# Kernel tuning notes

Measured on AMD Instinct MI355X. Metric: run time of the kernel, lower is better.

## Reference

```python
import jax, jax.numpy as jnp
import numpy as np
from jax import lax

TAU = 2.0
VTH = 1.0
T = 4

def heaviside(x):
    return (x >= 0.0).astype(x.dtype)

def lif_step(v, x):
    # decay_input=False, v_reset=0: v <- v*(1-1/tau) + x ; hard reset to 0
    v = v * (1.0 - 1.0 / TAU) + x
    s = heaviside(v - VTH)
    v = v * (1.0 - s)
    return v, s

def setup_inputs() -> dict:
    key = jax.random.key(0)
    k = jax.random.split(key, 5)
    B, H, W3, W4 = 128, 64, 8, 32
    cc, N, O = 8, 512, 16
    flat = cc * H * W3 * W4  # 131072
    x = jax.random.normal(k[0], (B, 2, H, W3, W4), dtype=jnp.float32)
    w_conv = jax.random.normal(k[1], (cc, 2, 3, 3), dtype=jnp.float32) / np.sqrt(2 * 9)
    w1 = jax.random.normal(k[2], (N, flat), dtype=jnp.float32) / np.sqrt(flat)
    w2 = jax.random.normal(k[3], (N, N), dtype=jnp.float32) / np.sqrt(N)
    w_out = jax.random.normal(k[4], (O, N), dtype=jnp.float32) / np.sqrt(N)
    return {"x": x, "w_conv": w_conv, "w1": w1, "w2": w2, "w_out": w_out}

def reference(x, w_conv, w1, w2, w_out):
    B = x.shape[0]
    # input.reshape(B, C, -1, W4)
    xr = x.reshape(B, x.shape[1], -1, x.shape[4])  # (B, 2, 512, 32)
    conv_input = lax.conv_general_dilated(
        xr, w_conv, window_strides=(1, 1), padding="SAME",
        dimension_numbers=("NCHW", "OIHW", "NCHW"))  # (B, cc, 512, 32)

    # lifconv applied T times to the same conv_input with persistent state
    def conv_step(v, _):
        return lif_step(v, conv_input)
    _, conv_spikes = lax.scan(conv_step, jnp.zeros_like(conv_input), None, length=T)  # (T,B,cc,H',W')

    N = w1.shape[0]
    def fc_step(carry, s_conv):
        v1, v2 = carry
        z1 = s_conv.reshape(B, -1) @ w1.T
        v1, s1 = lif_step(v1, z1)
        z2 = s1 @ w2.T
        v2, s2 = lif_step(v2, z2)
        return (v1, v2), (s1, s2)

    v0 = (jnp.zeros((B, N), x.dtype), jnp.zeros((B, N), x.dtype))
    _, (s1_rec, s2_rec) = lax.scan(fc_step, v0, conv_spikes)  # (T,B,N) each

    out = s2_rec.mean(axis=0) @ w_out.T  # (B, O)
    conv_spk_rec = jnp.moveaxis(conv_spikes, 0, 1)   # (B,T,cc,H',W')
    input_spk_rec = jnp.moveaxis(s1_rec, 0, 1)       # (B,T,N)
    hidden_spk_rec = jnp.moveaxis(s2_rec, 0, 1)      # (B,T,N)
    return (out, conv_spk_rec, input_spk_rec, hidden_spk_rec)
```

## Files before the change

kernel.cpp:

```cpp
#include <hip/hip_runtime.h>
#include <stdint.h>


#define OFF_CONV  2048ll
#define OFF_IN    67110912ll
#define OFF_HID   67373056ll

typedef short bf16x8 __attribute__((ext_vector_type(8)));
typedef float f32x4  __attribute__((ext_vector_type(4)));

__device__ __forceinline__ unsigned short f2bf(float f) {
  unsigned u = __float_as_uint(f);
  u += 0x7FFFu + ((u >> 16) & 1u);
  return (unsigned short)(u >> 16);
}

__device__ __forceinline__ void expand2(unsigned x, unsigned& o0, unsigned& o1) {
  o0 = (x & 1u) * 0x3F80u | (x & 0x100u) * 0x3F8000u;
  unsigned y = x >> 16;
  o1 = (y & 1u) * 0x3F80u | (y & 0x100u) * 0x3F8000u;
}

__global__ __launch_bounds__(256) void conv_lif_kernel(
    const float* __restrict__ x, const float* __restrict__ wc,
    float* __restrict__ out, unsigned char* __restrict__ patt)
{
  __shared__ float wcs[144];
  int tid = threadIdx.x;
  if (tid < 144) wcs[tid] = wc[tid];
  __syncthreads();

  int idx = blockIdx.x * 256 + tid;
  int b   = idx >> 15;
  int k4  = idx & 32767;
  int co  = k4 >> 12;
  int rem = k4 & 4095;
  int h   = rem >> 3;
  int w0  = (rem & 7) * 4;

  const float* xb = x + (long long)b * 32768;
  float c[4] = {0.f, 0.f, 0.f, 0.f};
#pragma unroll
  for (int ci = 0; ci < 2; ++ci) {
    const float* xc = xb + ci * 16384;
    const float* wk = wcs + co * 18 + ci * 9;
    float win[3][6];
#pragma unroll
    for (int r = 0; r < 3; ++r) {
      int hh = h - 1 + r;
      if (hh >= 0 && hh < 512) {
        const float* row = xc + hh * 32;
        float4 m = *(const float4*)(row + w0);
        win[r][1] = m.x; win[r][2] = m.y; win[r][3] = m.z; win[r][4] = m.w;
        win[r][0] = (w0 > 0)  ? row[w0 - 1] : 0.f;
        win[r][5] = (w0 < 28) ? row[w0 + 4] : 0.f;
      } else {
#pragma unroll
        for (int j = 0; j < 6; ++j) win[r][j] = 0.f;
      }
    }
#pragma unroll
    for (int r = 0; r < 3; ++r)
#pragma unroll
      for (int dw = 0; dw < 3; ++dw) {
        float wgt = wk[r * 3 + dw];
#pragma unroll
        for (int j = 0; j < 4; ++j) c[j] += win[r][j + dw] * wgt;
      }
  }

  int k = co * 16384 + h * 32 + w0;
  float* ob = out + OFF_CONV + (long long)b * 524288 + k;
  float v[4] = {0.f, 0.f, 0.f, 0.f};
  unsigned p[4] = {0, 0, 0, 0};
#pragma unroll
  for (int t = 0; t < 4; ++t) {
    f32x4 sv;
#pragma unroll
    for (int j = 0; j < 4; ++j) {
      v[j] = v[j] * 0.5f + c[j];
      int si = (v[j] >= 1.0f) ? 1 : 0;
      sv[j] = (float)si;
      if (si) v[j] = 0.f;
      p[j] |= (unsigned)si << t;
    }
    __builtin_nontemporal_store(sv, (f32x4*)(ob + t * 131072));
  }
  unsigned pb = p[0] | (p[1] << 8) | (p[2] << 16) | (p[3] << 24);
  *(unsigned*)(patt + (long long)b * 131072 + k) = pb;
}

__global__ __launch_bounds__(256) void transpose512(
    const float* __restrict__ w2, float* __restrict__ w2t)
{
  __shared__ float tile[32][33];
  int bx = blockIdx.x & 15, by = blockIdx.x >> 4;
  int tx = threadIdx.x & 31, ty = threadIdx.x >> 5;
#pragma unroll
  for (int i = 0; i < 32; i += 8)
    tile[ty + i][tx] = w2[(by * 32 + ty + i) * 512 + bx * 32 + tx];
  __syncthreads();
#pragma unroll
  for (int i = 0; i < 32; i += 8)
    w2t[(bx * 32 + ty + i) * 512 + by * 32 + tx] = tile[tx][ty + i];
}

__global__ __launch_bounds__(256, 2) void gemm_kernel(
    const unsigned char* __restrict__ patt, const float* __restrict__ w1,
    float* __restrict__ partials, int steps)
{
  __shared__ __attribute__((aligned(16))) unsigned char  AsP[128][48];
  __shared__ __attribute__((aligned(16))) unsigned short Bh[64][40];
  __shared__ __attribute__((aligned(16))) unsigned short Bl[64][40];

  const int tid   = threadIdx.x;
  const int S     = gridDim.x >> 3;
  const int nt    = blockIdx.x / S;
  const int chunk = blockIdx.x - nt * S;
  const long long k0 = (long long)chunk * steps * 32;

  const int ra  = tid >> 1;
  const int koa = (tid & 1) * 16;
  const unsigned char* pA = patt + (long long)ra * 131072 + k0 + koa;

  const int rb  = tid >> 2;
  const int kob = (tid & 3) * 8;
  const float* pB = w1 + (long long)(nt * 64 + rb) * 131072 + k0 + kob;

  const int lane = tid & 63;
  const int t    = tid >> 6;
  const int l15 = lane & 15, quad = lane >> 4;

  f32x4 acc[8][4];
#pragma unroll
  for (int i = 0; i < 8; ++i)
#pragma unroll
    for (int j = 0; j < 4; ++j) acc[i][j] = (f32x4){0.f, 0.f, 0.f, 0.f};

  uint4  pa  = *(const uint4*)pA;
  float4 fb0 = *(const float4*)pB;
  float4 fb1 = *(const float4*)(pB + 4);

  for (int s = 0; s < steps; ++s) {
    uint4 pan = pa; float4 f0n = fb0, f1n = fb1;
    if (s + 1 < steps) {
      pan = *(const uint4*)(pA + (long long)(s + 1) * 32);
      f0n = *(const float4*)(pB + (long long)(s + 1) * 32);
      f1n = *(const float4*)(pB + (long long)(s + 1) * 32 + 4);
    }

    *(uint4*)&AsP[ra][koa] = pa;

    {
      float fv[8] = {fb0.x, fb0.y, fb0.z, fb0.w, fb1.x, fb1.y, fb1.z, fb1.w};
      unsigned hp[4], lp[4];
#pragma unroll
      for (int i = 0; i < 4; ++i) {
        unsigned short h0 = f2bf(fv[2 * i]);
        unsigned short h1 = f2bf(fv[2 * i + 1]);
        float r0 = fv[2 * i]     - __uint_as_float((unsigned)h0 << 16);
        float r1 = fv[2 * i + 1] - __uint_as_float((unsigned)h1 << 16);
        hp[i] = (unsigned)h0 | ((unsigned)h1 << 16);
        lp[i] = (unsigned)f2bf(r0) | ((unsigned)f2bf(r1) << 16);
      }
      *(uint4*)&Bh[rb][kob] = make_uint4(hp[0], hp[1], hp[2], hp[3]);
      *(uint4*)&Bl[rb][kob] = make_uint4(lp[0], lp[1], lp[2], lp[3]);
    }

    __syncthreads();

    bf16x8 bh[4], bl[4];
#pragma unroll
    for (int fn = 0; fn < 4; ++fn) {
      bh[fn] = *(const bf16x8*)&Bh[fn * 16 + l15][quad * 8];
      bl[fn] = *(const bf16x8*)&Bl[fn * 16 + l15][quad * 8];
    }

    __builtin_amdgcn_s_setprio(1);
#pragma unroll
    for (int fm = 0; fm < 8; ++fm) {
      uint2 ap = *(const uint2*)&AsP[fm * 16 + l15][quad * 8];
      unsigned x0 = (ap.x >> t) & 0x01010101u;
      unsigned x1 = (ap.y >> t) & 0x01010101u;
      unsigned o0, o1, o2, o3;
      expand2(x0, o0, o1);
      expand2(x1, o2, o3);
      union { uint4 u; bf16x8 v; } au;
      au.u = make_uint4(o0, o1, o2, o3);
      bf16x8 a = au.v;
#pragma unroll
      for (int fn = 0; fn < 4; ++fn) {
        acc[fm][fn] = __builtin_amdgcn_mfma_f32_16x16x32_bf16(a, bh[fn], acc[fm][fn], 0, 0, 0);
        acc[fm][fn] = __builtin_amdgcn_mfma_f32_16x16x32_bf16(a, bl[fn], acc[fm][fn], 0, 0, 0);
      }
    }
    __builtin_amdgcn_s_setprio(0);

    __syncthreads();

    pa = pan; fb0 = f0n; fb1 = f1n;
  }

  float* pc = partials + (long long)chunk * 262144;
#pragma unroll
  for (int fm = 0; fm < 8; ++fm)
#pragma unroll
    for (int fn = 0; fn < 4; ++fn) {
      int m = t * 128 + fm * 16 + quad * 4;
      int n = nt * 64 + fn * 16 + l15;
#pragma unroll
      for (int rg = 0; rg < 4; ++rg)
        pc[(long long)(m + rg) * 512 + n] = acc[fm][fn][rg];
    }
}

__global__ __launch_bounds__(256) void reduce1_kernel(
    const float* __restrict__ partials, float* __restrict__ p2)
{
  int tg = blockIdx.x * 256 + threadIdx.x;
  int item = tg & 65535;
  int g = tg >> 16;
  const float* src = partials + (long long)g * 8 * 262144 + item * 4;
  float4 a = {0.f, 0.f, 0.f, 0.f};
#pragma unroll
  for (int c = 0; c < 8; ++c) {
    float4 p = *(const float4*)(src + (long long)c * 262144);
    a.x += p.x; a.y += p.y; a.z += p.z; a.w += p.w;
  }
  *(float4*)(p2 + (long long)g * 262144 + item * 4) = a;
}

__global__ __launch_bounds__(256) void reduce2_kernel(
    const float* __restrict__ p2, float* __restrict__ z1, int G)
{
  int item = blockIdx.x * 256 + threadIdx.x;
  float4 a = {0.f, 0.f, 0.f, 0.f};
  for (int g = 0; g < G; ++g) {
    float4 p = *(const float4*)(p2 + (long long)g * 262144 + item * 4);
    a.x += p.x; a.y += p.y; a.z += p.z; a.w += p.w;
  }
  *(float4*)(z1 + item * 4) = a;
}

__global__ __launch_bounds__(256) void reduce_kernel(
    const float* __restrict__ partials, float* __restrict__ z1, int S)
{
  int idx = (blockIdx.x * 256 + threadIdx.x) * 4;
  float4 a = {0.f, 0.f, 0.f, 0.f};
  for (int c = 0; c < S; ++c) {
    float4 p = *(const float4*)(partials + (long long)c * 262144 + idx);
    a.x += p.x; a.y += p.y; a.z += p.z; a.w += p.w;
  }
  *(float4*)(z1 + idx) = a;
}

__global__ __launch_bounds__(512) void fc_kernel(
    const float* __restrict__ z1, const float* __restrict__ w2t,
    const float* __restrict__ wout, float* __restrict__ out)
{
  int b = blockIdx.x;
  int n = threadIdx.x;
  __shared__ float s1s[512];
  __shared__ float red[512];
  __shared__ unsigned short idxs[512];
  __shared__ int cnts[8];

  const int wid = n >> 6, lane = n & 63;

  float v1 = 0.f, v2 = 0.f, ssum = 0.f;
#pragma unroll
  for (int t = 0; t < 4; ++t) {
    float z = z1[((t * 128 + b) << 9) + n];
    v1 = v1 * 0.5f + z;
    float s1 = (v1 >= 1.0f) ? 1.f : 0.f;
    out[OFF_IN + ((long long)b * 4 + t) * 512 + n] = s1;
    if (s1 != 0.f) v1 = 0.f;

    unsigned long long m = __ballot(s1 != 0.f);
    if (lane == 0) cnts[wid] = __popcll(m);
    __syncthreads();
    int base = 0, total = 0;
#pragma unroll
    for (int w = 0; w < 8; ++w) {
      int c = cnts[w];
      base  += (w < wid) ? c : 0;
      total += c;
    }
    if (s1 != 0.f) {
      int pos = base + (int)__popcll(m & ((1ull << lane) - 1ull));
      idxs[pos] = (unsigned short)n;
    }
    __syncthreads();

    float z2 = 0.f;
    int j = 0;
    for (; j + 8 <= total; j += 8) {
      float a0 = w2t[((int)idxs[j + 0] << 9) + n];
      float a1 = w2t[((int)idxs[j + 1] << 9) + n];
      float a2 = w2t[((int)idxs[j + 2] << 9) + n];
      float a3 = w2t[((int)idxs[j + 3] << 9) + n];
      float a4 = w2t[((int)idxs[j + 4] << 9) + n];
      float a5 = w2t[((int)idxs[j + 5] << 9) + n];
      float a6 = w2t[((int)idxs[j + 6] << 9) + n];
      float a7 = w2t[((int)idxs[j + 7] << 9) + n];
      z2 += a0; z2 += a1; z2 += a2; z2 += a3;
      z2 += a4; z2 += a5; z2 += a6; z2 += a7;
    }
    for (; j < total; ++j)
      z2 += w2t[((int)idxs[j] << 9) + n];

    v2 = v2 * 0.5f + z2;
    float s2 = (v2 >= 1.0f) ? 1.f : 0.f;
    out[OFF_HID + ((long long)b * 4 + t) * 512 + n] = s2;
    if (s2 != 0.f) v2 = 0.f;
    ssum += s2;
    __syncthreads();
  }

  s1s[n] = ssum * 0.25f;
  __syncthreads();

  int o = n & 15, part = n >> 4;
  float p = 0.f;
#pragma unroll
  for (int j = 0; j < 16; ++j)
    p += s1s[part * 16 + j] * wout[o * 512 + part * 16 + j];
  red[n] = p;
  __syncthreads();
  if (n < 16) {
    float a = 0.f;
#pragma unroll
    for (int pp = 0; pp < 32; ++pp) a += red[pp * 16 + n];
    out[b * 16 + n] = a;
  }
}

extern "C" void kernel_launch(void* const* d_in, const int* in_sizes, int n_in,
                              void* d_out, int out_size, void* d_ws, size_t ws_size,
                              hipStream_t stream) {
  const float* x     = (const float*)d_in[0];
  const float* wconv = (const float*)d_in[1];
  const float* w1    = (const float*)d_in[2];
  const float* w2    = (const float*)d_in[3];
  const float* wout  = (const float*)d_in[4];
  float* out = (float*)d_out;
  char* ws = (char*)d_ws;

  unsigned char* patt = (unsigned char*)ws;
  float* w2t      = (float*)(ws + 16777216);
  float* z1       = (float*)(ws + 16777216 + 1048576);
  float* partials = (float*)(ws + 16777216 + 2097152);
  float* p2       = (float*)ws;

  int S = 64;
  while (S > 1 && (size_t)(18874368ull + (size_t)S * 1048576ull) > ws_size) S >>= 1;
  int steps = 4096 / S;

  hipLaunchKernelGGL(conv_lif_kernel, dim3(16384), dim3(256), 0, stream,
                     x, wconv, out, patt);
  hipLaunchKernelGGL(transpose512, dim3(256), dim3(256), 0, stream, w2, w2t);
  hipLaunchKernelGGL(gemm_kernel, dim3(8 * S), dim3(256), 0, stream,
                     patt, w1, partials, steps);
  if (S >= 8) {
    int G = S / 8;
    hipLaunchKernelGGL(reduce1_kernel, dim3(G * 256), dim3(256), 0, stream,
                       partials, p2);
    hipLaunchKernelGGL(reduce2_kernel, dim3(256), dim3(256), 0, stream,
                       p2, z1, G);
  } else {
    hipLaunchKernelGGL(reduce_kernel, dim3(256), dim3(256), 0, stream,
                       partials, z1, S);
  }
  hipLaunchKernelGGL(fc_kernel, dim3(128), dim3(512), 0, stream,
                     z1, w2t, wout, out);
}
```

Before: 580.6 us.

## Double-buffer LDS tiles in GEMM and drop one barrier per step

Switches the main GEMM's shared-memory tiles (packed spikes A, bf16 hi/lo split of w1) to two buffers. Global loads now run two steps ahead, and the next tile is converted and staged while the current one feeds the MFMAs, so each iteration needs one barrier instead of two. In exchange the kernel uses twice the LDS and keeps extra prefetch registers, which may lower occupancy under launch_bounds(256,2) or cause spills.

```diff
diff --git a/kernel.cpp b/kernel.cpp
--- a/kernel.cpp
+++ b/kernel.cpp
@@ -109,9 +109,9 @@
     const unsigned char* __restrict__ patt, const float* __restrict__ w1,
     float* __restrict__ partials, int steps)
 {
-  __shared__ __attribute__((aligned(16))) unsigned char  AsP[128][48];
-  __shared__ __attribute__((aligned(16))) unsigned short Bh[64][40];
-  __shared__ __attribute__((aligned(16))) unsigned short Bl[64][40];
+  __shared__ __attribute__((aligned(16))) unsigned char  AsP[2][128][48];
+  __shared__ __attribute__((aligned(16))) unsigned short Bh[2][64][40];
+  __shared__ __attribute__((aligned(16))) unsigned short Bl[2][64][40];
 
   const int tid   = threadIdx.x;
   const int S     = gridDim.x >> 3;
@@ -137,49 +137,61 @@
 #pragma unroll
     for (int j = 0; j < 4; ++j) acc[i][j] = (f32x4){0.f, 0.f, 0.f, 0.f};
 
-  uint4  pa  = *(const uint4*)pA;
-  float4 fb0 = *(const float4*)pB;
-  float4 fb1 = *(const float4*)(pB + 4);
+  uint4 pa[2]; float4 f0[2], f1[2];
+
+#define STAGE(bb, PP, F0, F1)                                              \
+  {                                                                        \
+    *(uint4*)&AsP[bb][ra][koa] = (PP);                                     \
+    float fv[8] = {(F0).x, (F0).y, (F0).z, (F0).w,                         \
+                   (F1).x, (F1).y, (F1).z, (F1).w};                        \
+    unsigned hp[4], lp[4];                                                 \
+    _Pragma("unroll")                                                      \
+    for (int i = 0; i < 4; ++i) {                                          \
+      unsigned short h0 = f2bf(fv[2 * i]);                                 \
+      unsigned short h1 = f2bf(fv[2 * i + 1]);                             \
+      float r0 = fv[2 * i]     - __uint_as_float((unsigned)h0 << 16);      \
+      float r1 = fv[2 * i + 1] - __uint_as_float((unsigned)h1 << 16);      \
+      hp[i] = (unsigned)h0 | ((unsigned)h1 << 16);                         \
+      lp[i] = (unsigned)f2bf(r0) | ((unsigned)f2bf(r1) << 16);             \
+    }                                                                      \
+    *(uint4*)&Bh[bb][rb][kob] = make_uint4(hp[0], hp[1], hp[2], hp[3]);    \
+    *(uint4*)&Bl[bb][rb][kob] = make_uint4(lp[0], lp[1], lp[2], lp[3]);    \
+  }
+
+  pa[0] = *(const uint4*)pA;
+  f0[0] = *(const float4*)pB;
+  f1[0] = *(const float4*)(pB + 4);
+  STAGE(0, pa[0], f0[0], f1[0]);
+  if (steps > 1) {
+    pa[1] = *(const uint4*)(pA + 32);
+    f0[1] = *(const float4*)(pB + 32);
+    f1[1] = *(const float4*)(pB + 36);
+  }
+  __syncthreads();
 
   for (int s = 0; s < steps; ++s) {
-    uint4 pan = pa; float4 f0n = fb0, f1n = fb1;
-    if (s + 1 < steps) {
-      pan = *(const uint4*)(pA + (long long)(s + 1) * 32);
-      f0n = *(const float4*)(pB + (long long)(s + 1) * 32);
-      f1n = *(const float4*)(pB + (long long)(s + 1) * 32 + 4);
-    }
-
-    *(uint4*)&AsP[ra][koa] = pa;
-
-    {
-      float fv[8] = {fb0.x, fb0.y, fb0.z, fb0.w, fb1.x, fb1.y, fb1.z, fb1.w};
-      unsigned hp[4], lp[4];
-#pragma unroll
-      for (int i = 0; i < 4; ++i) {
-        unsigned short h0 = f2bf(fv[2 * i]);
-        unsigned short h1 = f2bf(fv[2 * i + 1]);
-        float r0 = fv[2 * i]     - __uint_as_float((unsigned)h0 << 16);
-        float r1 = fv[2 * i + 1] - __uint_as_float((unsigned)h1 << 16);
-        hp[i] = (unsigned)h0 | ((unsigned)h1 << 16);
-        lp[i] = (unsigned)f2bf(r0) | ((unsigned)f2bf(r1) << 16);
-      }
-      *(uint4*)&Bh[rb][kob] = make_uint4(hp[0], hp[1], hp[2], hp[3]);
-      *(uint4*)&Bl[rb][kob] = make_uint4(lp[0], lp[1], lp[2], lp[3]);
-    }
-
-    __syncthreads();
+    const int cur = s & 1;
+    const int nxt = (s + 1) & 1;
+
+    if (s + 2 < steps) {
+      pa[cur] = *(const uint4*)(pA + (long long)(s + 2) * 32);
+      f0[cur] = *(const float4*)(pB + (long long)(s + 2) * 32);
+      f1[cur] = *(const float4*)(pB + (long long)(s + 2) * 32 + 4);
+    }
+
+    if (s + 1 < steps) STAGE(nxt, pa[nxt], f0[nxt], f1[nxt]);
 
     bf16x8 bh[4], bl[4];
 #pragma unroll
     for (int fn = 0; fn < 4; ++fn) {
-      bh[fn] = *(const bf16x8*)&Bh[fn * 16 + l15][quad * 8];
-      bl[fn] = *(const bf16x8*)&Bl[fn * 16 + l15][quad * 8];
+      bh[fn] = *(const bf16x8*)&Bh[cur][fn * 16 + l15][quad * 8];
+      bl[fn] = *(const bf16x8*)&Bl[cur][fn * 16 + l15][quad * 8];
     }
 
     __builtin_amdgcn_s_setprio(1);
 #pragma unroll
     for (int fm = 0; fm < 8; ++fm) {
-      uint2 ap = *(const uint2*)&AsP[fm * 16 + l15][quad * 8];
+      uint2 ap = *(const uint2*)&AsP[cur][fm * 16 + l15][quad * 8];
       unsigned x0 = (ap.x >> t) & 0x01010101u;
       unsigned x1 = (ap.y >> t) & 0x01010101u;
       unsigned o0, o1, o2, o3;
@@ -197,9 +209,8 @@
     __builtin_amdgcn_s_setprio(0);
 
     __syncthreads();
-
-    pa = pan; fb0 = f0n; fb1 = f1n;
-  }
+  }
+#undef STAGE
 
   float* pc = partials + (long long)chunk * 262144;
 #pragma unroll
```

After: 690.6 us. 1.19x slower.
